# Kernel optimization log

Hardware: AMD Instinct MI355X
Metric: run time of the kernel (lower is better)

Reference implementation:

```python
import jax, jax.numpy as jnp
import numpy as np

EPS = 1e-6
TEMPERATURE = 0.1
NEG_INF = -1.0e9

B, S, H = 8, 1024, 1024
M = 16384  # memory_size


def setup_inputs() -> dict:
    key = jax.random.key(0)
    ks = jax.random.split(key, 10)
    sc = 1.0 / np.sqrt(H)
    return {
        "hidden_states": jax.random.normal(ks[0], (B, S, H), jnp.float32),
        "Wk": jax.random.normal(ks[1], (H, H), jnp.float32) * sc,
        "bk": jax.random.normal(ks[2], (H,), jnp.float32) * 0.01,
        "Wv": jax.random.normal(ks[3], (H, H), jnp.float32) * sc,
        "bv": jax.random.normal(ks[4], (H,), jnp.float32) * 0.01,
        "Wo": jax.random.normal(ks[5], (H, H), jnp.float32) * sc,
        "bo": jax.random.normal(ks[6], (H,), jnp.float32) * 0.01,
        "memory_keys": jax.random.normal(ks[7], (M, H), jnp.float32),
        "memory_values": jax.random.normal(ks[8], (M, H), jnp.float32),
        "memory_usage": jax.random.randint(ks[9], (M,), 0, 3, jnp.int32),
    }


def _normalize(x):
    # matches torch: x * rsqrt(sum(x^2) + 1e-6)
    return x * jax.lax.rsqrt(jnp.sum(jnp.square(x), axis=-1, keepdims=True) + EPS)


def reference(hidden_states, Wk, bk, Wv, bv, Wo, bo,
              memory_keys, memory_values, memory_usage):
    # key projection + L2-ish normalization of queries
    q = hidden_states @ Wk.T + bk              # [B,S,H]
    qn = _normalize(q)
    mkn = _normalize(memory_keys)              # [M,H]
    # cosine-similarity attention over memory slots
    scores = jnp.einsum('bsh,mh->bsm', qn, mkn) / TEMPERATURE  # [B,S,M]
    mask = (memory_usage > 0).astype(scores.dtype)             # [M]
    scores = scores * mask + NEG_INF * (1.0 - mask)
    w = jax.nn.softmax(scores, axis=-1)                        # [B,S,M]
    retrieved = jnp.einsum('bsm,mh->bsh', w, memory_values)    # [B,S,H]
    return retrieved @ Wo.T + bo
```

## Files before the change

### kernel.cpp

```cpp
#include <hip/hip_runtime.h>
#include <hip/hip_bf16.h>
#include <stdint.h>
#include <stddef.h>

typedef __bf16 bf16_t;
typedef __attribute__((ext_vector_type(8))) __bf16 bf16x8;
typedef __attribute__((ext_vector_type(4))) __bf16 bf16x4;
typedef __attribute__((ext_vector_type(4))) float f32x4;

#define HDIM 1024
#define MSLOTS 16384
#define NROWS 8192
#define KSPL 8

__device__ __forceinline__ void load16_lds(const void* g, void* l) {
  __builtin_amdgcn_global_load_lds((const __attribute__((address_space(1))) void*)g,
                                   (__attribute__((address_space(3))) void*)l, 16, 0, 0);
}

__global__ void init_compact(int* __restrict__ cmask) {
  int i = blockIdx.x * blockDim.x + threadIdx.x;
  if (i < MSLOTS) cmask[i] = 0;
}

__global__ void compact_scan(const int* __restrict__ usage, int* __restrict__ posmap,
                             int* __restrict__ cmask, int* __restrict__ smalls) {
  __shared__ int wtot[16], wbase[16];
  const int t = threadIdx.x;
  const int lane = t & 63, wid = t >> 6;
  const int base = t * 16;
  unsigned mask = 0;
  int c = 0;
  #pragma unroll
  for (int i = 0; i < 16; ++i) {
    if (usage[base + i] > 0) { mask |= (1u << i); ++c; }
  }
  int inc = c;
  #pragma unroll
  for (int d = 1; d < 64; d <<= 1) {
    int n = __shfl_up(inc, d);
    if (lane >= d) inc += n;
  }
  if (lane == 63) wtot[wid] = inc;
  __syncthreads();
  if (t == 0) {
    int acc = 0;
    #pragma unroll
    for (int w = 0; w < 16; ++w) { wbase[w] = acc; acc += wtot[w]; }
    smalls[0] = acc;
    smalls[1] = ((acc + 511) >> 9) << 9;
  }
  __syncthreads();
  int pos = wbase[wid] + inc - c;
  #pragma unroll
  for (int i = 0; i < 16; ++i) {
    if ((mask >> i) & 1u) {
      posmap[pos] = base + i;
      cmask[pos] = 1;
      ++pos;
    }
  }
}

__global__ void cvt_f32_bf16(const float* __restrict__ X, bf16_t* __restrict__ Y, int n8) {
  int i = blockIdx.x * blockDim.x + threadIdx.x;
  if (i >= n8) return;
  float4 a = ((const float4*)X)[2 * i];
  float4 b = ((const float4*)X)[2 * i + 1];
  bf16x8 o;
  o[0] = (bf16_t)a.x; o[1] = (bf16_t)a.y; o[2] = (bf16_t)a.z; o[3] = (bf16_t)a.w;
  o[4] = (bf16_t)b.x; o[5] = (bf16_t)b.y; o[6] = (bf16_t)b.z; o[7] = (bf16_t)b.w;
  ((bf16x8*)Y)[i] = o;
}

__global__ void normalize_rows(const float* __restrict__ X, bf16_t* __restrict__ Y) {
  __shared__ float part[4];
  const int t = threadIdx.x;
  const size_t row = blockIdx.x;
  float4 v = ((const float4*)(X + row * 1024))[t];
  float s = v.x * v.x + v.y * v.y + v.z * v.z + v.w * v.w;
  #pragma unroll
  for (int m = 32; m >= 1; m >>= 1) s += __shfl_xor(s, m);
  if ((t & 63) == 0) part[t >> 6] = s;
  __syncthreads();
  float tot = part[0] + part[1] + part[2] + part[3];
  float r = rsqrtf(tot + 1e-6f);
  bf16x4 o;
  o[0] = (bf16_t)(v.x * r); o[1] = (bf16_t)(v.y * r);
  o[2] = (bf16_t)(v.z * r); o[3] = (bf16_t)(v.w * r);
  *(bf16x4*)&Y[row * 1024 + t * 4] = o;
}

__global__ void normalize_gather(const float* __restrict__ mk, const int* __restrict__ posmap,
                                 const int* __restrict__ smalls, bf16_t* __restrict__ cmkn) {
  __shared__ float part[4];
  const int p = blockIdx.x;
  const int cnt = smalls[0], mpad = smalls[1];
  if (p >= mpad) return;
  const int t = threadIdx.x;
  if (p >= cnt) {
    bf16x4 z;
    z[0] = z[1] = z[2] = z[3] = (bf16_t)0.f;
    *(bf16x4*)&cmkn[(size_t)p * 1024 + t * 4] = z;
    return;
  }
  const int slot = posmap[p];
  float4 v = ((const float4*)(mk + (size_t)slot * 1024))[t];
  float s = v.x * v.x + v.y * v.y + v.z * v.z + v.w * v.w;
  #pragma unroll
  for (int m = 32; m >= 1; m >>= 1) s += __shfl_xor(s, m);
  if ((t & 63) == 0) part[t >> 6] = s;
  __syncthreads();
  float tot = part[0] + part[1] + part[2] + part[3];
  float r = rsqrtf(tot + 1e-6f);
  bf16x4 o;
  o[0] = (bf16_t)(v.x * r); o[1] = (bf16_t)(v.y * r);
  o[2] = (bf16_t)(v.z * r); o[3] = (bf16_t)(v.w * r);
  *(bf16x4*)&cmkn[(size_t)p * 1024 + t * 4] = o;
}

__global__ void transpose_gather(const float* __restrict__ mv, const int* __restrict__ posmap,
                                 const int* __restrict__ smalls, bf16_t* __restrict__ cVt) {
  __shared__ float tile[32][33];
  const int cnt = smalls[0], mpad = smalls[1];
  const int p0 = blockIdx.y * 32;
  if (p0 >= mpad) return;
  const int tx = threadIdx.x & 31, ty = threadIdx.x >> 5;
  const int h0 = blockIdx.x * 32;
  #pragma unroll
  for (int j = 0; j < 32; j += 8) {
    const int pos = p0 + ty + j;
    float val = 0.f;
    if (pos < cnt) val = mv[(size_t)posmap[pos] * 1024 + h0 + tx];
    tile[ty + j][tx] = val;
  }
  __syncthreads();
  #pragma unroll
  for (int j = 0; j < 32; j += 8)
    cVt[(size_t)(h0 + ty + j) * MSLOTS + p0 + tx] = (bf16_t)tile[tx][ty + j];
}

__global__ void zero_f32(float* __restrict__ p, int n4) {
  int i = blockIdx.x * blockDim.x + threadIdx.x;
  if (i < n4) ((float4*)p)[i] = (float4){0.f, 0.f, 0.f, 0.f};
}

__global__ void scale_cvt(const float* __restrict__ retrf, const float* __restrict__ den,
                          bf16_t* __restrict__ out, int n4) {
  int i = blockIdx.x * blockDim.x + threadIdx.x;
  if (i >= n4) return;
  float4 s = ((const float4*)retrf)[i];
  const int row = (i * 4) >> 10;
  const float r = 1.0f / den[row];
  bf16x4 o;
  o[0] = (bf16_t)(s.x * r); o[1] = (bf16_t)(s.y * r);
  o[2] = (bf16_t)(s.z * r); o[3] = (bf16_t)(s.w * r);
  ((bf16x4*)out)[i] = o;
}

template <int EPI>
__global__ void gemm_bt(const bf16_t* __restrict__ A, const bf16_t* __restrict__ Bt,
                        int ldk, int kLenIn, int ldc,
                        const float* __restrict__ bias,
                        const int* __restrict__ cmask,
                        float* __restrict__ den,
                        float* __restrict__ outf, bf16_t* __restrict__ outb,
                        const int* __restrict__ smalls, int ks) {
  __shared__ bf16_t lA[128 * 32];
  __shared__ bf16_t lB[128 * 32];
  const int t = threadIdx.x;
  const int lane = t & 63;
  const int wave = t >> 6;
  const int wm = (wave >> 1) << 6;
  const int wn = (wave & 1) << 6;
  const int lr = lane & 15;
  const int lq = lane >> 4;

  int bx = blockIdx.x, by = blockIdx.y, bz = blockIdx.z;
  int kLen = kLenIn;
  int kstart = 0;
  if (EPI == 1) {
    if (bx * 128 >= smalls[1]) return;
  }
  if (EPI == 3) {
    const unsigned nx = gridDim.x, ny = gridDim.y;
    if ((ny & 7u) == 0u) {
      unsigned lin = blockIdx.x + nx * (blockIdx.y + ny * blockIdx.z);
      unsigned ylow = lin & 7u;
      unsigned rest = lin >> 3;
      bx = rest % nx;
      unsigned rest2 = rest / nx;
      unsigned yhigh = rest2 % (ny >> 3);
      bz = rest2 / (ny >> 3);
      by = ylow + 8u * yhigh;
    }
    kLen = smalls[1] / ks;
    kstart = bz * kLen;
  }

  const int r0 = t >> 2;
  const int c0 = (t & 3) * 8;
  const bf16_t* pA0 = A + (size_t)(by * 128 + r0) * ldk + kstart + c0;
  const bf16_t* pA1 = pA0 + (size_t)64 * ldk;
  const bf16_t* pB0 = Bt + (size_t)(bx * 128 + r0) * ldk + kstart + c0;
  const bf16_t* pB1 = pB0 + (size_t)64 * ldk;

  f32x4 acc[4][4];
  #pragma unroll
  for (int i = 0; i < 4; ++i)
    #pragma unroll
    for (int j = 0; j < 4; ++j) acc[i][j] = (f32x4){0.f, 0.f, 0.f, 0.f};

  for (int k0 = 0; k0 < kLen; k0 += 32) {
    __syncthreads();
    load16_lds(pA0, &lA[t * 8]);
    load16_lds(pA1, &lA[2048 + t * 8]);
    load16_lds(pB0, &lB[t * 8]);
    load16_lds(pB1, &lB[2048 + t * 8]);
    pA0 += 32; pA1 += 32; pB0 += 32; pB1 += 32;
    __syncthreads();
    bf16x8 af[4], bfr[4];
    #pragma unroll
    for (int i = 0; i < 4; ++i)
      af[i] = *(const bf16x8*)&lA[(wm + i * 16 + lr) * 32 + lq * 8];
    #pragma unroll
    for (int j = 0; j < 4; ++j)
      bfr[j] = *(const bf16x8*)&lB[(wn + j * 16 + lr) * 32 + lq * 8];
    #pragma unroll
    for (int i = 0; i < 4; ++i)
      #pragma unroll
      for (int j = 0; j < 4; ++j)
        acc[i][j] = __builtin_amdgcn_mfma_f32_16x16x32_bf16(af[i], bfr[j], acc[i][j], 0, 0, 0);
  }

  const int colBase = bx * 128 + wn + lr;
  const int rowBase = by * 128 + wm + lq * 4;

  float rs[4][4];
  if (EPI == 1) {
    #pragma unroll
    for (int i = 0; i < 4; ++i)
      #pragma unroll
      for (int r = 0; r < 4; ++r) rs[i][r] = 0.f;
  }

  #pragma unroll
  for (int j = 0; j < 4; ++j) {
    const int col = colBase + j * 16;
    float bval = 0.f;
    bool ok = true;
    if (EPI == 0) bval = bias[col];
    if (EPI == 1) ok = cmask[col] > 0;
    #pragma unroll
    for (int i = 0; i < 4; ++i) {
      const int row = rowBase + i * 16;
      #pragma unroll
      for (int r = 0; r < 4; ++r) {
        const size_t idx = (size_t)(row + r) * ldc + col;
        float v = acc[i][j][r];
        if (EPI == 0) outf[idx] = v + bval;
        if (EPI == 1) {
          float e = ok ? exp2f(v * 14.426950408889634f) : 0.f;
          rs[i][r] += e;
          outb[idx] = (bf16_t)e;
        }
        if (EPI == 3) atomicAdd(&outf[idx], v);
      }
    }
  }

  if (EPI == 1) {
    #pragma unroll
    for (int i = 0; i < 4; ++i)
      #pragma unroll
      for (int r = 0; r < 4; ++r) {
        float s = rs[i][r];
        s += __shfl_xor(s, 1);
        s += __shfl_xor(s, 2);
        s += __shfl_xor(s, 4);
        s += __shfl_xor(s, 8);
        if (lr == 0) atomicAdd(&den[rowBase + i * 16 + r], s);
      }
  }
}

extern "C" void kernel_launch(void* const* d_in, const int* in_sizes, int n_in,
                              void* d_out, int out_size, void* d_ws, size_t ws_size,
                              hipStream_t stream) {
  const float* hs = (const float*)d_in[0];
  const float* Wk = (const float*)d_in[1];
  const float* bk = (const float*)d_in[2];
  const float* Wo = (const float*)d_in[5];
  const float* bo = (const float*)d_in[6];
  const float* mk = (const float*)d_in[7];
  const float* mv = (const float*)d_in[8];
  const int* usage = (const int*)d_in[9];
  float* out = (float*)d_out;

  char* ws = (char*)d_ws;
  size_t off = 0;
  auto alloc = [&](size_t b) -> void* {
    void* p = ws + off;
    off += (b + 255) & ~(size_t)255;
    return p;
  };
  bf16_t* cmkn = (bf16_t*)alloc((size_t)MSLOTS * HDIM * 2);
  bf16_t* cVt = (bf16_t*)alloc((size_t)HDIM * MSLOTS * 2);
  bf16_t* qnb = (bf16_t*)alloc((size_t)NROWS * HDIM * 2);
  bf16_t* retrb = (bf16_t*)alloc((size_t)NROWS * HDIM * 2);
  bf16_t* Wob = (bf16_t*)alloc((size_t)HDIM * HDIM * 2);
  float* den = (float*)alloc((size_t)NROWS * 4);
  int* posmap = (int*)alloc((size_t)MSLOTS * 4);
  int* cmask = (int*)alloc((size_t)MSLOTS * 4);
  int* smalls = (int*)alloc(256 * 4);
  const size_t fixed = off;

  int chunk = 128;
  {
    const int cc[7] = {8192, 4096, 2048, 1024, 512, 256, 128};
    for (int ci = 0; ci < 7; ++ci) {
      size_t region = (size_t)cc[ci] * (MSLOTS * 2 + HDIM * 4);
      size_t phaseA = (size_t)NROWS * HDIM * 2 + (size_t)HDIM * HDIM * 2 +
                      (size_t)NROWS * HDIM * 4 + 1024;
      if (region < phaseA) region = phaseA;
      if (fixed + region <= ws_size) { chunk = cc[ci]; break; }
    }
  }
  bf16_t* hsb = (bf16_t*)(ws + fixed);
  bf16_t* Wkb = (bf16_t*)(ws + fixed + (size_t)NROWS * HDIM * 2);
  float* qf = (float*)(ws + fixed + (size_t)NROWS * HDIM * 2 + (size_t)HDIM * HDIM * 2);
  bf16_t* P = (bf16_t*)(ws + fixed);
  float* retrf = (float*)(ws + fixed + (size_t)chunk * MSLOTS * 2);

  init_compact<<<MSLOTS / 256, 256, 0, stream>>>(cmask);
  compact_scan<<<1, 1024, 0, stream>>>(usage, posmap, cmask, smalls);
  cvt_f32_bf16<<<(NROWS * HDIM / 8 + 255) / 256, 256, 0, stream>>>(hs, hsb, NROWS * HDIM / 8);
  cvt_f32_bf16<<<(HDIM * HDIM / 8 + 255) / 256, 256, 0, stream>>>(Wk, Wkb, HDIM * HDIM / 8);
  cvt_f32_bf16<<<(HDIM * HDIM / 8 + 255) / 256, 256, 0, stream>>>(Wo, Wob, HDIM * HDIM / 8);
  normalize_gather<<<MSLOTS, 256, 0, stream>>>(mk, posmap, smalls, cmkn);
  transpose_gather<<<dim3(HDIM / 32, MSLOTS / 32), 256, 0, stream>>>(mv, posmap, smalls, cVt);

  gemm_bt<0><<<dim3(HDIM / 128, NROWS / 128), 256, 0, stream>>>(
      hsb, Wkb, HDIM, HDIM, HDIM, bk, nullptr, nullptr, qf, nullptr, smalls, 1);
  normalize_rows<<<NROWS, 256, 0, stream>>>(qf, qnb);

  for (int c = 0; c < NROWS; c += chunk) {
    zero_f32<<<(chunk / 4 + 255) / 256, 256, 0, stream>>>(den, chunk / 4);
    zero_f32<<<(chunk * HDIM / 4 + 255) / 256, 256, 0, stream>>>(retrf, chunk * HDIM / 4);
    gemm_bt<1><<<dim3(MSLOTS / 128, chunk / 128), 256, 0, stream>>>(
        qnb + (size_t)c * HDIM, cmkn, HDIM, HDIM, MSLOTS, nullptr, cmask, den, nullptr, P,
        smalls, 1);
    gemm_bt<3><<<dim3(HDIM / 128, chunk / 128, KSPL), 256, 0, stream>>>(
        P, cVt, MSLOTS, 0, HDIM, nullptr, nullptr, nullptr, retrf, nullptr, smalls, KSPL);
    scale_cvt<<<(chunk * HDIM / 4 + 255) / 256, 256, 0, stream>>>(
        retrf, den, retrb + (size_t)c * HDIM, chunk * HDIM / 4);
  }

  gemm_bt<0><<<dim3(HDIM / 128, NROWS / 128), 256, 0, stream>>>(
      retrb, Wob, HDIM, HDIM, HDIM, bo, nullptr, nullptr, out, nullptr, smalls, 1);
}
```

Baseline: 963.5 us.

## Replace atomic split-K accumulation with partial buffers plus fused reduce-scale

Adds a split-K mode where each K slice of the P·V GEMM writes plain stores into its own partial buffer. A new reduce_scale kernel then sums the partials and applies the softmax denominator. This removes the zeroing pass and the float atomics, and the chunk/ksplit choice now depends on available workspace. The grouped block-index swizzle is also applied to every GEMM variant rather than only the split-K one. The cost is extra workspace and a read of ksplit partial buffers in the reduction.

```diff
diff --git a/kernel.cpp b/kernel.cpp
--- a/kernel.cpp
+++ b/kernel.cpp
@@ -11,7 +11,6 @@
 #define HDIM 1024
 #define MSLOTS 16384
 #define NROWS 8192
-#define KSPL 8
 
 __device__ __forceinline__ void load16_lds(const void* g, void* l) {
   __builtin_amdgcn_global_load_lds((const __attribute__((address_space(1))) void*)g,
@@ -158,6 +157,23 @@
   ((bf16x4*)out)[i] = o;
 }
 
+__global__ void reduce_scale(const float* __restrict__ part, size_t partStride, int ks,
+                             const float* __restrict__ den, bf16_t* __restrict__ out, int n4) {
+  int i = blockIdx.x * blockDim.x + threadIdx.x;
+  if (i >= n4) return;
+  float4 s = ((const float4*)part)[i];
+  for (int k = 1; k < ks; ++k) {
+    float4 t = ((const float4*)(part + (size_t)k * partStride))[i];
+    s.x += t.x; s.y += t.y; s.z += t.z; s.w += t.w;
+  }
+  const int row = (i * 4) >> 10;
+  const float r = 1.0f / den[row];
+  bf16x4 o;
+  o[0] = (bf16_t)(s.x * r); o[1] = (bf16_t)(s.y * r);
+  o[2] = (bf16_t)(s.z * r); o[3] = (bf16_t)(s.w * r);
+  ((bf16x4*)out)[i] = o;
+}
+
 template <int EPI>
 __global__ void gemm_bt(const bf16_t* __restrict__ A, const bf16_t* __restrict__ Bt,
                         int ldk, int kLenIn, int ldc,
@@ -165,7 +181,7 @@
                         const int* __restrict__ cmask,
                         float* __restrict__ den,
                         float* __restrict__ outf, bf16_t* __restrict__ outb,
-                        const int* __restrict__ smalls, int ks) {
+                        const int* __restrict__ smalls, int ks, size_t partStride) {
   __shared__ bf16_t lA[128 * 32];
   __shared__ bf16_t lB[128 * 32];
   const int t = threadIdx.x;
@@ -177,23 +193,26 @@
   const int lq = lane >> 4;
 
   int bx = blockIdx.x, by = blockIdx.y, bz = blockIdx.z;
+  {
+    const unsigned nx = gridDim.x, ny = gridDim.y;
+    if ((ny & 7u) == 0u) {
+      unsigned lin = blockIdx.x + nx * (blockIdx.y + ny * blockIdx.z);
+      unsigned ylow = lin & 7u;
+      lin >>= 3;
+      bx = lin % nx;
+      lin /= nx;
+      unsigned yhigh = lin % (ny >> 3);
+      bz = lin / (ny >> 3);
+      by = ylow + 8u * yhigh;
+    }
+  }
+
   int kLen = kLenIn;
   int kstart = 0;
   if (EPI == 1) {
     if (bx * 128 >= smalls[1]) return;
   }
-  if (EPI == 3) {
-    const unsigned nx = gridDim.x, ny = gridDim.y;
-    if ((ny & 7u) == 0u) {
-      unsigned lin = blockIdx.x + nx * (blockIdx.y + ny * blockIdx.z);
-      unsigned ylow = lin & 7u;
-      unsigned rest = lin >> 3;
-      bx = rest % nx;
-      unsigned rest2 = rest / nx;
-      unsigned yhigh = rest2 % (ny >> 3);
-      bz = rest2 / (ny >> 3);
-      by = ylow + 8u * yhigh;
-    }
+  if (EPI == 3 || EPI == 4) {
     kLen = smalls[1] / ks;
     kstart = bz * kLen;
   }
@@ -235,6 +254,8 @@
 
   const int colBase = bx * 128 + wn + lr;
   const int rowBase = by * 128 + wm + lq * 4;
+
+  if (EPI == 4) outf += (size_t)bz * partStride;
 
   float rs[4][4];
   if (EPI == 1) {
@@ -265,6 +286,7 @@
           outb[idx] = (bf16_t)e;
         }
         if (EPI == 3) atomicAdd(&outf[idx], v);
+        if (EPI == 4) outf[idx] = v;
       }
     }
   }
@@ -315,15 +337,21 @@
   int* smalls = (int*)alloc(256 * 4);
   const size_t fixed = off;
 
-  int chunk = 128;
+  int chunk = 128, ksplit = 4, partialMode = 0;
   {
-    const int cc[7] = {8192, 4096, 2048, 1024, 512, 256, 128};
-    for (int ci = 0; ci < 7; ++ci) {
-      size_t region = (size_t)cc[ci] * (MSLOTS * 2 + HDIM * 4);
+    const int cc[8] = {4096, 4096, 2048, 2048, 1024, 1024, 512, 128};
+    const int kk[8] = {4, 4, 8, 8, 8, 8, 16, 4};
+    const int pp[8] = {1, 0, 1, 0, 1, 0, 0, 0};
+    for (int ci = 0; ci < 8; ++ci) {
+      size_t outBytes = pp[ci] ? (size_t)cc[ci] * HDIM * 4 * kk[ci] : (size_t)cc[ci] * HDIM * 4;
+      size_t region = (size_t)cc[ci] * MSLOTS * 2 + outBytes;
       size_t phaseA = (size_t)NROWS * HDIM * 2 + (size_t)HDIM * HDIM * 2 +
                       (size_t)NROWS * HDIM * 4 + 1024;
       if (region < phaseA) region = phaseA;
-      if (fixed + region <= ws_size) { chunk = cc[ci]; break; }
+      if (fixed + region <= ws_size) {
+        chunk = cc[ci]; ksplit = kk[ci]; partialMode = pp[ci];
+        break;
+      }
     }
   }
   bf16_t* hsb = (bf16_t*)(ws + fixed);
@@ -331,6 +359,7 @@
   float* qf = (float*)(ws + fixed + (size_t)NROWS * HDIM * 2 + (size_t)HDIM * HDIM * 2);
   bf16_t* P = (bf16_t*)(ws + fixed);
   float* retrf = (float*)(ws + fixed + (size_t)chunk * MSLOTS * 2);
+  const size_t partStride = (size_t)chunk * HDIM;
 
   init_compact<<<MSLOTS / 256, 256, 0, stream>>>(cmask);
   compact_scan<<<1, 1024, 0, stream>>>(usage, posmap, cmask, smalls);
@@ -341,21 +370,30 @@
   transpose_gather<<<dim3(HDIM / 32, MSLOTS / 32), 256, 0, stream>>>(mv, posmap, smalls, cVt);
 
   gemm_bt<0><<<dim3(HDIM / 128, NROWS / 128), 256, 0, stream>>>(
-      hsb, Wkb, HDIM, HDIM, HDIM, bk, nullptr, nullptr, qf, nullptr, smalls, 1);
+      hsb, Wkb, HDIM, HDIM, HDIM, bk, nullptr, nullptr, qf, nullptr, smalls, 1, 0);
   normalize_rows<<<NROWS, 256, 0, stream>>>(qf, qnb);
 
   for (int c = 0; c < NROWS; c += chunk) {
     zero_f32<<<(chunk / 4 + 255) / 256, 256, 0, stream>>>(den, chunk / 4);
-    zero_f32<<<(chunk * HDIM / 4 + 255) / 256, 256, 0, stream>>>(retrf, chunk * HDIM / 4);
     gemm_bt<1><<<dim3(MSLOTS / 128, chunk / 128), 256, 0, stream>>>(
         qnb + (size_t)c * HDIM, cmkn, HDIM, HDIM, MSLOTS, nullptr, cmask, den, nullptr, P,
-        smalls, 1);
-    gemm_bt<3><<<dim3(HDIM / 128, chunk / 128, KSPL), 256, 0, stream>>>(
-        P, cVt, MSLOTS, 0, HDIM, nullptr, nullptr, nullptr, retrf, nullptr, smalls, KSPL);
-    scale_cvt<<<(chunk * HDIM / 4 + 255) / 256, 256, 0, stream>>>(
-        retrf, den, retrb + (size_t)c * HDIM, chunk * HDIM / 4);
+        smalls, 1, 0);
+    if (partialMode) {
+      gemm_bt<4><<<dim3(HDIM / 128, chunk / 128, ksplit), 256, 0, stream>>>(
+          P, cVt, MSLOTS, 0, HDIM, nullptr, nullptr, nullptr, retrf, nullptr, smalls, ksplit,
+          partStride);
+      reduce_scale<<<(chunk * HDIM / 4 + 255) / 256, 256, 0, stream>>>(
+          retrf, partStride, ksplit, den, retrb + (size_t)c * HDIM, chunk * HDIM / 4);
+    } else {
+      zero_f32<<<(chunk * HDIM / 4 + 255) / 256, 256, 0, stream>>>(retrf, chunk * HDIM / 4);
+      gemm_bt<3><<<dim3(HDIM / 128, chunk / 128, ksplit), 256, 0, stream>>>(
+          P, cVt, MSLOTS, 0, HDIM, nullptr, nullptr, nullptr, retrf, nullptr, smalls, ksplit,
+          0);
+      scale_cvt<<<(chunk * HDIM / 4 + 255) / 256, 256, 0, stream>>>(
+          retrf, den, retrb + (size_t)c * HDIM, chunk * HDIM / 4);
+    }
   }
 
   gemm_bt<0><<<dim3(HDIM / 128, NROWS / 128), 256, 0, stream>>>(
-      retrb, Wob, HDIM, HDIM, HDIM, bo, nullptr, nullptr, out, nullptr, smalls, 1);
-}
+      retrb, Wob, HDIM, HDIM, HDIM, bo, nullptr, nullptr, out, nullptr, smalls, 1, 0);
+}
```

After: 892.6 us. -7.4%, faster.
